# Kernel tuning notes

Measured on AMD Instinct MI355X. Metric: run time of the kernel, lower is better.

Reference implementation:

```python
import jax, jax.numpy as jnp
import numpy as np

HEADS = 8
DIM_HEAD = 64
SCALE = DIM_HEAD ** -0.5  # q scaling
EPS = 1e-5  # channel LayerNorm eps (float32)


def setup_inputs() -> dict:
    key = jax.random.key(0)
    ks = jax.random.split(key, 4)
    B, C, H, W = 8, 256, 64, 64
    hd = HEADS * DIM_HEAD  # 512
    x = jax.random.normal(ks[0], (B, C, H, W), dtype=jnp.float32)
    w_qkv = jax.random.normal(ks[1], (3 * hd, C), dtype=jnp.float32) * 0.02  # 1x1 conv, no bias
    w_out = jax.random.normal(ks[2], (C, hd), dtype=jnp.float32) * 0.02     # 1x1 conv
    b_out = jax.random.normal(ks[3], (C,), dtype=jnp.float32) * 0.02
    g_ln = jnp.ones((C,), dtype=jnp.float32)  # LayerNorm gamma
    return {"x": x, "w_qkv": w_qkv, "w_out": w_out, "b_out": b_out, "g_ln": g_ln}


def reference(x, w_qkv, w_out, b_out, g_ln):
    B, C, H, W = x.shape
    n = H * W
    hd = HEADS * DIM_HEAD
    # 1x1 conv == per-pixel matmul: [B,C,H,W] x [3hd,C] -> [B,3hd,H,W]
    qkv = jnp.einsum('bchw,oc->bohw', x, w_qkv).reshape(B, 3, HEADS, DIM_HEAD, n)
    q, k, v = qkv[:, 0], qkv[:, 1], qkv[:, 2]  # each [B,h,d,n]
    q = jax.nn.softmax(q, axis=-2) * SCALE      # softmax over head-dim d
    k = jax.nn.softmax(k, axis=-1)              # softmax over spatial n
    v = v / n
    context = jnp.einsum('bhdn,bhen->bhde', k, v)   # [B,h,d,e]
    out = jnp.einsum('bhde,bhdn->bhen', context, q)  # [B,h,e,n]
    out = out.reshape(B, hd, H, W)
    # to_out: 1x1 conv + bias, then channel-wise LayerNorm (gamma only)
    y = jnp.einsum('bchw,oc->bohw', out, w_out) + b_out[None, :, None, None]
    mean = jnp.mean(y, axis=1, keepdims=True)
    var = jnp.var(y, axis=1, keepdims=True)  # unbiased=False
    return (y - mean) * jax.lax.rsqrt(var + EPS) * g_ln[None, :, None, None]
```

## Files before the change

### kernel.cpp

```cpp
#include <hip/hip_runtime.h>
#include <stdint.h>


#define NB    8
#define CCH   256
#define NSP   4096
#define O3    1536
#define NH    8
#define DH    64
#define CSTR  136

typedef unsigned short u16;
typedef unsigned int   u32;
typedef __bf16 bf16;
typedef bf16  bf16x8 __attribute__((ext_vector_type(8)));
typedef float f32x4  __attribute__((ext_vector_type(4)));
typedef u16   u16x8  __attribute__((ext_vector_type(8)));
typedef u16   u16x4  __attribute__((ext_vector_type(4)));

__device__ __forceinline__ float b2f(u16 h) {
  union { u32 u; float f; } x; x.u = ((u32)h) << 16; return x.f;
}
__device__ __forceinline__ u16 f2b(float f) {
  union { float f; u32 u; } x; x.f = f;
  u32 r = x.u + 0x7fffu + ((x.u >> 16) & 1u);
  return (u16)(r >> 16);
}
__device__ __forceinline__ int detect_bf(const void* g) {
  return ((const u32*)g)[0] != 0x3F800000u;
}
__device__ __forceinline__ void ldg2lds16(const u16* g, u16* l) {
  __builtin_amdgcn_global_load_lds((const __attribute__((address_space(1))) void*)g,
                                   (__attribute__((address_space(3))) void*)l,
                                   16, 0, 0);
}

#define TSTR 68
__global__ __launch_bounds__(256) void k_prep(const void* __restrict__ xv,
                                              const void* __restrict__ wv,
                                              u16* __restrict__ xT,
                                              u16* __restrict__ Wb,
                                              float* __restrict__ S,
                                              const void* __restrict__ g_lnv) {
  const int isbf = detect_bf(g_lnv);
  const int t = threadIdx.x;
  if (blockIdx.z == 8) {
    const int tid = blockIdx.y * 64 + blockIdx.x;
    if (tid < 192) {
      const int idx = tid * 256 + t;
      const int row = idx >> 5, cu = idx & 31;
      int nr;
      if (row < 512)       nr = row;
      else if (row < 1024) nr = 512 + ((row - 512) >> 6) * 128 + (row & 63);
      else                 nr = 512 + ((row - 1024) >> 6) * 128 + 64 + (row & 63);
      const int didx = nr * 32 + cu;
      if (isbf) {
        reinterpret_cast<uint4*>(Wb)[didx] = reinterpret_cast<const uint4*>(wv)[idx];
      } else {
        float4 a = reinterpret_cast<const float4*>(wv)[idx * 2];
        float4 b = reinterpret_cast<const float4*>(wv)[idx * 2 + 1];
        ushort4 o0, o1;
        o0.x = f2b(a.x); o0.y = f2b(a.y); o0.z = f2b(a.z); o0.w = f2b(a.w);
        o1.x = f2b(b.x); o1.y = f2b(b.y); o1.z = f2b(b.z); o1.w = f2b(b.w);
        reinterpret_cast<ushort4*>(Wb)[didx * 2]     = o0;
        reinterpret_cast<ushort4*>(Wb)[didx * 2 + 1] = o1;
      }
    } else if (tid < 200) {
      reinterpret_cast<float2*>(S)[(tid - 192) * 256 + t] = (float2){0.f, 0.f};
    }
    return;
  }
  const int b = blockIdx.z, cb = blockIdx.y * 64, nb = blockIdx.x * 64;
  __shared__ u16 tile[64 * TSTR];
  if (isbf) {
    const u16* xb = (const u16*)xv;
#pragma unroll
    for (int rr = 0; rr < 2; ++rr) {
      const int u = t + 256 * rr;
      const int c = u >> 3, ch = u & 7;
      u16x8 v = *reinterpret_cast<const u16x8*>(
          xb + ((size_t)(b * CCH + cb + c) * NSP + nb + ch * 8));
      u16* dst = tile + c * TSTR + ch * 8;
      *reinterpret_cast<u16x4*>(dst)     = (u16x4){v[0], v[1], v[2], v[3]};
      *reinterpret_cast<u16x4*>(dst + 4) = (u16x4){v[4], v[5], v[6], v[7]};
    }
  } else {
    const float* xb = (const float*)xv;
#pragma unroll
    for (int rr = 0; rr < 4; ++rr) {
      const int u = t + 256 * rr;
      const int c = u >> 4, c4 = u & 15;
      float4 f = *reinterpret_cast<const float4*>(
          xb + ((size_t)(b * CCH + cb + c) * NSP + nb + c4 * 4));
      u16x4 o; o[0] = f2b(f.x); o[1] = f2b(f.y); o[2] = f2b(f.z); o[3] = f2b(f.w);
      *reinterpret_cast<u16x4*>(tile + c * TSTR + c4 * 4) = o;
    }
  }
  __syncthreads();
#pragma unroll
  for (int rr = 0; rr < 2; ++rr) {
    const int u = t + 256 * rr;
    const int n = u >> 3, cc = u & 7;
    u16x8 o;
#pragma unroll
    for (int e = 0; e < 8; ++e) o[e] = tile[(cc * 8 + e) * TSTR + n];
    *reinterpret_cast<u16x8*>(
        xT + ((size_t)(b * NSP + nb + n) * CCH + cb + cc * 8)) = o;
  }
}

__global__ __launch_bounds__(256) void k_kv_mfma(const u16* __restrict__ Wb,
                                                 const u16* __restrict__ xT,
                                                 float* __restrict__ S,
                                                 float* __restrict__ ctxp) {
  __shared__ __align__(16) u16 pool[64 * CSTR * 2];
  u16* As = pool;
  u16* Bs = pool + 4096;
  u16* ekS = pool;
  u16* vS  = pool + 64 * CSTR;

  const int b = blockIdx.z, h = blockIdx.y, n0 = blockIdx.x * 128;
  const int m0 = 512 + h * 128;
  const int t = threadIdx.x, w = t >> 6, l = t & 63;
  const int wm = (w >> 1) * 64, wn = (w & 1) * 64;
  const int fr = l & 15, quad = l >> 4;

  f32x4 acc[4][4];
#pragma unroll
  for (int i = 0; i < 4; ++i)
#pragma unroll
    for (int j = 0; j < 4; ++j) acc[i][j] = (f32x4){0.f, 0.f, 0.f, 0.f};

  {
    const u16* A = Wb;
    const u16* B = xT + (size_t)b * NSP * CCH;
    const int s0 = w * 2, s1 = s0 + 1;
    const int ra0 = s0 * 16 + (l >> 2);
    const int ra1 = s1 * 16 + (l >> 2);
    const int kc  = (l & 3) * 8;
    const int fq  = quad * 8;
    for (int k0 = 0; k0 < 256; k0 += 32) {
      ldg2lds16(A + (size_t)(m0 + ra0) * 256 + k0 + kc, As + s0 * 512);
      ldg2lds16(A + (size_t)(m0 + ra1) * 256 + k0 + kc, As + s1 * 512);
      ldg2lds16(B + (size_t)(n0 + ra0) * 256 + k0 + kc, Bs + s0 * 512);
      ldg2lds16(B + (size_t)(n0 + ra1) * 256 + k0 + kc, Bs + s1 * 512);
      asm volatile("s_waitcnt vmcnt(0)" ::: "memory");
      __syncthreads();
      bf16x8 af[4], bg[4];
#pragma unroll
      for (int i = 0; i < 4; ++i)
        af[i] = *reinterpret_cast<const bf16x8*>(As + (wm + i * 16 + fr) * 32 + fq);
#pragma unroll
      for (int j = 0; j < 4; ++j)
        bg[j] = *reinterpret_cast<const bf16x8*>(Bs + (wn + j * 16 + fr) * 32 + fq);
#pragma unroll
      for (int i = 0; i < 4; ++i)
#pragma unroll
        for (int j = 0; j < 4; ++j)
          acc[i][j] = __builtin_amdgcn_mfma_f32_16x16x32_bf16(af[i], bg[j], acc[i][j], 0, 0, 0);
      __syncthreads();
    }
  }

  {
    u16* dstT = (w < 2) ? ekS : vS;
#pragma unroll
    for (int i = 0; i < 4; ++i)
#pragma unroll
      for (int r = 0; r < 4; ++r) {
        const int row = i * 16 + quad * 4 + r;
#pragma unroll
        for (int j = 0; j < 4; ++j) {
          float v = acc[i][j][r];
          if (w < 2) v = __expf(v);
          dstT[row * CSTR + wn + j * 16 + fr] = f2b(v);
        }
      }
  }
  __syncthreads();

  {
    const int d = t >> 2, seg = t & 3;
    float s = 0.f;
    const u16* src = ekS + d * CSTR + seg * 32;
#pragma unroll
    for (int m = 0; m < 32; ++m) s += b2f(src[m]);
    s += __shfl_xor(s, 1);
    s += __shfl_xor(s, 2);
    if ((t & 3) == 0) atomicAdd(&S[b * 512 + h * 64 + d], s);
  }

  f32x4 c2[4];
#pragma unroll
  for (int j = 0; j < 4; ++j) c2[j] = (f32x4){0.f, 0.f, 0.f, 0.f};
#pragma unroll
  for (int k0 = 0; k0 < 128; k0 += 32) {
    bf16x8 af = *reinterpret_cast<const bf16x8*>(ekS + (w * 16 + fr) * CSTR + k0 + quad * 8);
#pragma unroll
    for (int j = 0; j < 4; ++j) {
      bf16x8 bg = *reinterpret_cast<const bf16x8*>(vS + (j * 16 + fr) * CSTR + k0 + quad * 8);
      c2[j] = __builtin_amdgcn_mfma_f32_16x16x32_bf16(af, bg, c2[j], 0, 0, 0);
    }
  }
  float* cb = ctxp + ((size_t)blockIdx.x * 64 + b * NH + h) * 4096;
#pragma unroll
  for (int j = 0; j < 4; ++j)
#pragma unroll
    for (int r = 0; r < 4; ++r)
      cb[(w * 16 + quad * 4 + r) * 64 + j * 16 + fr] = c2[j][r];
}

__global__ __launch_bounds__(256) void k_fold(const float* __restrict__ ctxp,
                                              const void* __restrict__ w_outv,
                                              const float* __restrict__ S,
                                              u16* __restrict__ Mb,
                                              const void* __restrict__ g_lnv) {
  const int isbf = detect_bf(g_lnv);
  const int h = blockIdx.x, b = blockIdx.y, ds = blockIdx.z * 16;
  const int t = threadIdx.x;
  __shared__ float ctxS[16][64];
  __shared__ float invS[16];
  if (t < 16) invS[t] = (1.0f / 4096.0f) / S[b * 512 + h * 64 + ds + t];
  const size_t bhoff = (size_t)(b * NH + h) * 4096 + (size_t)ds * 64;
#pragma unroll
  for (int i = 0; i < 4; ++i) {
    const int idx = t + 256 * i;
    float s = 0.f;
#pragma unroll
    for (int ch = 0; ch < 32; ++ch)
      s += ctxp[(size_t)ch * 64 * 4096 + bhoff + idx];
    ctxS[idx >> 6][idx & 63] = s;
  }
  float wrow[64];
  if (isbf) {
    const u16* wsrc = (const u16*)w_outv + (size_t)t * 512 + h * DH;
#pragma unroll
    for (int e4 = 0; e4 < 64; e4 += 4) {
      ushort4 u = *reinterpret_cast<const ushort4*>(wsrc + e4);
      wrow[e4 + 0] = b2f(u.x); wrow[e4 + 1] = b2f(u.y);
      wrow[e4 + 2] = b2f(u.z); wrow[e4 + 3] = b2f(u.w);
    }
  } else {
    const float* wsrc = (const float*)w_outv + (size_t)t * 512 + h * DH;
#pragma unroll
    for (int e4 = 0; e4 < 64; e4 += 4) {
      float4 f = *reinterpret_cast<const float4*>(wsrc + e4);
      wrow[e4 + 0] = f.x; wrow[e4 + 1] = f.y;
      wrow[e4 + 2] = f.z; wrow[e4 + 3] = f.w;
    }
  }
  __syncthreads();
  u16* dst = Mb + ((size_t)(b * CCH + t)) * 512 + h * DH + ds;
  for (int d = 0; d < 16; ++d) {
    float s = 0.f;
#pragma unroll
    for (int e = 0; e < 64; e += 4) {
      float4 c4 = *reinterpret_cast<const float4*>(&ctxS[d][e]);
      s += wrow[e] * c4.x + wrow[e + 1] * c4.y + wrow[e + 2] * c4.z + wrow[e + 3] * c4.w;
    }
    dst[d] = f2b(s * invS[d]);
  }
}

__global__ __launch_bounds__(512) void k_qmq_ln(const u16* __restrict__ Wb,
                                                const u16* __restrict__ xT,
                                                const u16* __restrict__ Mb,
                                                const void* __restrict__ b_outv,
                                                const void* __restrict__ g_lnv,
                                                void* __restrict__ outv) {
  __shared__ __align__(16) u16 qS[64 * 512];
  __shared__ __align__(16) u16 pool[18432];
  __shared__ float redS[8][4][16];
  __shared__ float redQ[8][4][16];
  __shared__ float gS[256], bS[256];

  const int isbf = detect_bf(g_lnv);
  const int b  = blockIdx.y;
  const int n0 = blockIdx.x * 64;
  const int t  = threadIdx.x, w = t >> 6, l = t & 63;
  const int fr = l & 15, quad = l >> 4;
  const int kcs = (((l & 3) ^ ((l >> 3) & 3)) * 8);
  const int fsw = (quad ^ ((fr >> 1) & 3)) * 8;

  if (t < 256) {
    gS[t] = isbf ? b2f(((const u16*)g_lnv)[t]) : ((const float*)g_lnv)[t];
    bS[t] = isbf ? b2f(((const u16*)b_outv)[t]) : ((const float*)b_outv)[t];
  }

  {
    u16* As = pool;
    u16* Bs = pool + 16384;
    f32x4 qa[4][4];
#pragma unroll
    for (int i = 0; i < 4; ++i)
#pragma unroll
      for (int j = 0; j < 4; ++j) qa[i][j] = (f32x4){0.f, 0.f, 0.f, 0.f};

    const u16* Bg = xT + (size_t)b * NSP * CCH;
    for (int k0 = 0; k0 < 256; k0 += 32) {
#pragma unroll
      for (int s = 0; s < 4; ++s) {
        const int row = w * 64 + s * 16 + (l >> 2);
        ldg2lds16(Wb + (size_t)row * 256 + k0 + kcs, As + (w * 64 + s * 16) * 32);
      }
      if (w < 4) {
        const int row = w * 16 + (l >> 2);
        ldg2lds16(Bg + (size_t)(n0 + row) * 256 + k0 + kcs, Bs + (w * 16) * 32);
      }
      asm volatile("s_waitcnt vmcnt(0)" ::: "memory");
      __syncthreads();
      bf16x8 af[4], bg[4];
#pragma unroll
      for (int i = 0; i < 4; ++i)
        af[i] = *reinterpret_cast<const bf16x8*>(As + (w * 64 + i * 16 + fr) * 32 + fsw);
#pragma unroll
      for (int j = 0; j < 4; ++j)
        bg[j] = *reinterpret_cast<const bf16x8*>(Bs + (j * 16 + fr) * 32 + fsw);
#pragma unroll
      for (int i = 0; i < 4; ++i)
#pragma unroll
        for (int j = 0; j < 4; ++j)
          qa[i][j] = __builtin_amdgcn_mfma_f32_16x16x32_bf16(af[i], bg[j], qa[i][j], 0, 0, 0);
      __syncthreads();
    }

#pragma unroll
    for (int j = 0; j < 4; ++j) {
      float s = 0.f;
#pragma unroll
      for (int i = 0; i < 4; ++i)
#pragma unroll
        for (int r = 0; r < 4; ++r) { qa[i][j][r] = __expf(qa[i][j][r]); s += qa[i][j][r]; }
      s += __shfl_xor(s, 16);
      s += __shfl_xor(s, 32);
      const float inv = 0.125f / s;
      const int n   = j * 16 + fr;
      const int swz = (n & 7) << 4;
#pragma unroll
      for (int i = 0; i < 4; ++i) {
        ushort4 o;
        o.x = f2b(qa[i][j][0] * inv); o.y = f2b(qa[i][j][1] * inv);
        o.z = f2b(qa[i][j][2] * inv); o.w = f2b(qa[i][j][3] * inv);
        const int hd2 = (w * 64 + i * 16 + quad * 4) * 2;
        *reinterpret_cast<ushort4*>(
            reinterpret_cast<char*>(qS) + ((n * 1024 + hd2) ^ swz)) = o;
      }
    }
  }
  __syncthreads();

  f32x4 acc[2][4];
#pragma unroll
  for (int i = 0; i < 2; ++i)
#pragma unroll
    for (int j = 0; j < 4; ++j) acc[i][j] = (f32x4){0.f, 0.f, 0.f, 0.f};

  {
    u16* Am = pool;
    const u16* Ag = Mb + (size_t)b * CCH * 512;
    for (int k0 = 0; k0 < 512; k0 += 32) {
#pragma unroll
      for (int s = 0; s < 2; ++s) {
        const int row = w * 32 + s * 16 + (l >> 2);
        ldg2lds16(Ag + (size_t)row * 512 + k0 + kcs, Am + (w * 32 + s * 16) * 32);
      }
      asm volatile("s_waitcnt vmcnt(0)" ::: "memory");
      __syncthreads();
      bf16x8 af[2], bg[4];
#pragma unroll
      for (int i = 0; i < 2; ++i)
        af[i] = *reinterpret_cast<const bf16x8*>(Am + (w * 32 + i * 16 + fr) * 32 + fsw);
#pragma unroll
      for (int j = 0; j < 4; ++j) {
        const int n = j * 16 + fr;
        const int byteoff = (n * 1024 + k0 * 2 + quad * 16) ^ ((n & 7) << 4);
        bg[j] = *reinterpret_cast<const bf16x8*>(
            reinterpret_cast<const char*>(qS) + byteoff);
      }
#pragma unroll
      for (int i = 0; i < 2; ++i)
#pragma unroll
        for (int j = 0; j < 4; ++j)
          acc[i][j] = __builtin_amdgcn_mfma_f32_16x16x32_bf16(af[i], bg[j], acc[i][j], 0, 0, 0);
      __syncthreads();
    }
  }

  float ps[4] = {}, pq[4] = {};
#pragma unroll
  for (int i = 0; i < 2; ++i)
#pragma unroll
    for (int r = 0; r < 4; ++r) {
      const int c = w * 32 + i * 16 + quad * 4 + r;
      const float bi = bS[c];
#pragma unroll
      for (int j = 0; j < 4; ++j) {
        acc[i][j][r] += bi;
        ps[j] += acc[i][j][r];
        pq[j] += acc[i][j][r] * acc[i][j][r];
      }
    }
#pragma unroll
  for (int j = 0; j < 4; ++j) {
    ps[j] += __shfl_xor(ps[j], 16); ps[j] += __shfl_xor(ps[j], 32);
    pq[j] += __shfl_xor(pq[j], 16); pq[j] += __shfl_xor(pq[j], 32);
  }
  if (quad == 0) {
#pragma unroll
    for (int j = 0; j < 4; ++j) { redS[w][j][fr] = ps[j]; redQ[w][j][fr] = pq[j]; }
  }
  __syncthreads();
  float mean[4], inv[4];
#pragma unroll
  for (int j = 0; j < 4; ++j) {
    float s = 0.f, q = 0.f;
#pragma unroll
    for (int g = 0; g < 8; ++g) { s += redS[g][j][fr]; q += redQ[g][j][fr]; }
    const float mn = s * (1.0f / 256.0f);
    const float vr = q * (1.0f / 256.0f) - mn * mn;
    mean[j] = mn;
    inv[j] = rsqrtf(vr + 1e-5f);
  }

#pragma unroll
  for (int i = 0; i < 2; ++i)
#pragma unroll
    for (int r = 0; r < 4; ++r) {
      const int c = w * 32 + i * 16 + quad * 4 + r;
      const float g = gS[c];
#pragma unroll
      for (int j = 0; j < 4; ++j) {
        const int col = n0 + j * 16 + fr;
        const float o = (acc[i][j][r] - mean[j]) * inv[j] * g;
        const size_t idx = ((size_t)b * CCH + c) * NSP + col;
        if (isbf) ((u16*)outv)[idx] = f2b(o);
        else      ((float*)outv)[idx] = o;
      }
    }
}

extern "C" void kernel_launch(void* const* d_in, const int* in_sizes, int n_in,
                              void* d_out, int out_size, void* d_ws, size_t ws_size,
                              hipStream_t stream) {
  (void)in_sizes; (void)n_in; (void)out_size; (void)ws_size;
  const void* x     = d_in[0];
  const void* w_qkv = d_in[1];
  const void* w_out = d_in[2];
  const void* b_out = d_in[3];
  const void* g_ln  = d_in[4];

  char* ws = (char*)d_ws;
  u16*   Wb   = (u16*)(ws + 256);
  float* S    = (float*)(ws + 851968);
  u16*   xT   = (u16*)(ws + 1048576);
  float* ctxp = (float*)(ws + 17825792);
  u16*   Mb   = (u16*)(ws + 51380224);

  k_prep    <<<dim3(64, 4, 9),  256, 0, stream>>>(x, w_qkv, xT, Wb, S, g_ln);
  k_kv_mfma <<<dim3(32, NH, NB),256, 0, stream>>>(Wb, xT, S, ctxp);
  k_fold    <<<dim3(NH, NB, 4), 256, 0, stream>>>(ctxp, w_out, S, Mb, g_ln);
  k_qmq_ln  <<<dim3(64, NB),    512, 0, stream>>>(Wb, xT, Mb, b_out, g_ln, d_out);
}
```

Baseline: 176.9 us.

## Double-buffer LDS tiles in both GEMM phases and prefetch second-phase operand

Doubles the shared pool so the q-projection GEMM and the context GEMM each double-buffer their global-to-LDS tiles, using partial vmcnt waits so the next tile's loads overlap the current tile's MFMAs. The second GEMM's K step grows from 32 to 64 with a new XOR swizzle, and its first tile is issued before the softmax epilogue so that load overlaps the exp/normalize work. The larger LDS footprint may lower occupancy, and the hand-counted vmcnt values and raw s_barrier calls have to match the number of outstanding loads exactly.

Measured after the change: 171.3 us. 3.2% less time.

```diff
diff --git a/kernel.cpp b/kernel.cpp
--- a/kernel.cpp
+++ b/kernel.cpp
@@ -269,7 +269,7 @@
                                                 const void* __restrict__ g_lnv,
                                                 void* __restrict__ outv) {
   __shared__ __align__(16) u16 qS[64 * 512];
-  __shared__ __align__(16) u16 pool[18432];
+  __shared__ __align__(16) u16 pool[36864];
   __shared__ float redS[8][4][16];
   __shared__ float redQ[8][4][16];
   __shared__ float gS[256], bS[256];
@@ -287,64 +287,98 @@
     bS[t] = isbf ? b2f(((const u16*)b_outv)[t]) : ((const float*)b_outv)[t];
   }
 
+  const u16* Bg = xT + (size_t)b * NSP * CCH;
+  const u16* Ag = Mb + (size_t)b * CCH * 512;
+
+  f32x4 qa[4][4];
+#pragma unroll
+  for (int i = 0; i < 4; ++i)
+#pragma unroll
+    for (int j = 0; j < 4; ++j) qa[i][j] = (f32x4){0.f, 0.f, 0.f, 0.f};
+
   {
-    u16* As = pool;
-    u16* Bs = pool + 16384;
-    f32x4 qa[4][4];
-#pragma unroll
-    for (int i = 0; i < 4; ++i)
-#pragma unroll
-      for (int j = 0; j < 4; ++j) qa[i][j] = (f32x4){0.f, 0.f, 0.f, 0.f};
-
-    const u16* Bg = xT + (size_t)b * NSP * CCH;
-    for (int k0 = 0; k0 < 256; k0 += 32) {
+    {
+      u16* As0 = pool; u16* Bs0 = pool + 16384;
 #pragma unroll
       for (int s = 0; s < 4; ++s) {
         const int row = w * 64 + s * 16 + (l >> 2);
-        ldg2lds16(Wb + (size_t)row * 256 + k0 + kcs, As + (w * 64 + s * 16) * 32);
+        ldg2lds16(Wb + (size_t)row * 256 + kcs, As0 + (w * 64 + s * 16) * 32);
       }
       if (w < 4) {
-        const int row = w * 16 + (l >> 2);
-        ldg2lds16(Bg + (size_t)(n0 + row) * 256 + k0 + kcs, Bs + (w * 16) * 32);
-      }
-      asm volatile("s_waitcnt vmcnt(0)" ::: "memory");
-      __syncthreads();
+        const int row = n0 + w * 16 + (l >> 2);
+        ldg2lds16(Bg + (size_t)row * 256 + kcs, Bs0 + (w * 16) * 32);
+      }
+    }
+    int cur = 0;
+    for (int k0 = 0; k0 < 256; k0 += 32) {
+      const int last = (k0 + 32 >= 256);
+      if (!last) {
+        u16* Asn = pool + (cur ^ 1) * 18432;
+        u16* Bsn = Asn + 16384;
+        const int kn = k0 + 32;
+#pragma unroll
+        for (int s = 0; s < 4; ++s) {
+          const int row = w * 64 + s * 16 + (l >> 2);
+          ldg2lds16(Wb + (size_t)row * 256 + kn + kcs, Asn + (w * 64 + s * 16) * 32);
+        }
+        if (w < 4) {
+          const int row = n0 + w * 16 + (l >> 2);
+          ldg2lds16(Bg + (size_t)row * 256 + kn + kcs, Bsn + (w * 16) * 32);
+        }
+        if (w < 4) asm volatile("s_waitcnt vmcnt(5)" ::: "memory");
+        else       asm volatile("s_waitcnt vmcnt(4)" ::: "memory");
+      } else {
+        asm volatile("s_waitcnt vmcnt(0)" ::: "memory");
+      }
+      __builtin_amdgcn_s_barrier();
+      const u16* Asc = pool + cur * 18432;
+      const u16* Bsc = Asc + 16384;
       bf16x8 af[4], bg[4];
 #pragma unroll
       for (int i = 0; i < 4; ++i)
-        af[i] = *reinterpret_cast<const bf16x8*>(As + (w * 64 + i * 16 + fr) * 32 + fsw);
+        af[i] = *reinterpret_cast<const bf16x8*>(Asc + (w * 64 + i * 16 + fr) * 32 + fsw);
 #pragma unroll
       for (int j = 0; j < 4; ++j)
-        bg[j] = *reinterpret_cast<const bf16x8*>(Bs + (j * 16 + fr) * 32 + fsw);
+        bg[j] = *reinterpret_cast<const bf16x8*>(Bsc + (j * 16 + fr) * 32 + fsw);
 #pragma unroll
       for (int i = 0; i < 4; ++i)
 #pragma unroll
         for (int j = 0; j < 4; ++j)
           qa[i][j] = __builtin_amdgcn_mfma_f32_16x16x32_bf16(af[i], bg[j], qa[i][j], 0, 0, 0);
-      __syncthreads();
-    }
-
-#pragma unroll
-    for (int j = 0; j < 4; ++j) {
-      float s = 0.f;
-#pragma unroll
-      for (int i = 0; i < 4; ++i)
-#pragma unroll
-        for (int r = 0; r < 4; ++r) { qa[i][j][r] = __expf(qa[i][j][r]); s += qa[i][j][r]; }
-      s += __shfl_xor(s, 16);
-      s += __shfl_xor(s, 32);
-      const float inv = 0.125f / s;
-      const int n   = j * 16 + fr;
-      const int swz = (n & 7) << 4;
-#pragma unroll
-      for (int i = 0; i < 4; ++i) {
-        ushort4 o;
-        o.x = f2b(qa[i][j][0] * inv); o.y = f2b(qa[i][j][1] * inv);
-        o.z = f2b(qa[i][j][2] * inv); o.w = f2b(qa[i][j][3] * inv);
-        const int hd2 = (w * 64 + i * 16 + quad * 4) * 2;
-        *reinterpret_cast<ushort4*>(
-            reinterpret_cast<char*>(qS) + ((n * 1024 + hd2) ^ swz)) = o;
-      }
+      __builtin_amdgcn_s_barrier();
+      cur ^= 1;
+    }
+  }
+
+  {
+    const int srck = ((l & 7) ^ ((l >> 3) & 7)) * 8;
+#pragma unroll
+    for (int s = 0; s < 4; ++s) {
+      const int r0 = w * 32 + s * 8;
+      ldg2lds16(Ag + (size_t)(r0 + (l >> 3)) * 512 + srck, pool + r0 * 64);
+    }
+  }
+
+#pragma unroll
+  for (int j = 0; j < 4; ++j) {
+    float s = 0.f;
+#pragma unroll
+    for (int i = 0; i < 4; ++i)
+#pragma unroll
+      for (int r = 0; r < 4; ++r) { qa[i][j][r] = __expf(qa[i][j][r]); s += qa[i][j][r]; }
+    s += __shfl_xor(s, 16);
+    s += __shfl_xor(s, 32);
+    const float inv = 0.125f / s;
+    const int n   = j * 16 + fr;
+    const int swz = (n & 7) << 4;
+#pragma unroll
+    for (int i = 0; i < 4; ++i) {
+      ushort4 o;
+      o.x = f2b(qa[i][j][0] * inv); o.y = f2b(qa[i][j][1] * inv);
+      o.z = f2b(qa[i][j][2] * inv); o.w = f2b(qa[i][j][3] * inv);
+      const int hd2 = (w * 64 + i * 16 + quad * 4) * 2;
+      *reinterpret_cast<ushort4*>(
+          reinterpret_cast<char*>(qS) + ((n * 1024 + hd2) ^ swz)) = o;
     }
   }
   __syncthreads();
@@ -356,33 +390,53 @@
     for (int j = 0; j < 4; ++j) acc[i][j] = (f32x4){0.f, 0.f, 0.f, 0.f};
 
   {
-    u16* Am = pool;
-    const u16* Ag = Mb + (size_t)b * CCH * 512;
-    for (int k0 = 0; k0 < 512; k0 += 32) {
-#pragma unroll
-      for (int s = 0; s < 2; ++s) {
-        const int row = w * 32 + s * 16 + (l >> 2);
-        ldg2lds16(Ag + (size_t)row * 512 + k0 + kcs, Am + (w * 32 + s * 16) * 32);
-      }
-      asm volatile("s_waitcnt vmcnt(0)" ::: "memory");
-      __syncthreads();
-      bf16x8 af[2], bg[4];
-#pragma unroll
-      for (int i = 0; i < 2; ++i)
-        af[i] = *reinterpret_cast<const bf16x8*>(Am + (w * 32 + i * 16 + fr) * 32 + fsw);
+    const int srck = ((l & 7) ^ ((l >> 3) & 7)) * 8;
+    int cur = 0;
+    for (int k0 = 0; k0 < 512; k0 += 64) {
+      const int last = (k0 + 64 >= 512);
+      if (!last) {
+        u16* Amn = pool + (cur ^ 1) * 16384;
+        const int kn = k0 + 64;
+#pragma unroll
+        for (int s = 0; s < 4; ++s) {
+          const int r0 = w * 32 + s * 8;
+          ldg2lds16(Ag + (size_t)(r0 + (l >> 3)) * 512 + kn + srck, Amn + r0 * 64);
+        }
+        asm volatile("s_waitcnt vmcnt(4)" ::: "memory");
+      } else {
+        asm volatile("s_waitcnt vmcnt(0)" ::: "memory");
+      }
+      __builtin_amdgcn_s_barrier();
+      const u16* Amc = pool + cur * 16384;
+      bf16x8 af0[2], af1[2], bg0[4], bg1[4];
+      const int c0 = (quad ^ (fr & 7)) * 8;
+      const int c1 = ((4 + quad) ^ (fr & 7)) * 8;
+#pragma unroll
+      for (int i = 0; i < 2; ++i) {
+        const int rb = (w * 32 + i * 16 + fr) * 64;
+        af0[i] = *reinterpret_cast<const bf16x8*>(Amc + rb + c0);
+        af1[i] = *reinterpret_cast<const bf16x8*>(Amc + rb + c1);
+      }
 #pragma unroll
       for (int j = 0; j < 4; ++j) {
         const int n = j * 16 + fr;
-        const int byteoff = (n * 1024 + k0 * 2 + quad * 16) ^ ((n & 7) << 4);
-        bg[j] = *reinterpret_cast<const bf16x8*>(
-            reinterpret_cast<const char*>(qS) + byteoff);
+        const int o0 = (n * 1024 + k0 * 2 + quad * 16) ^ ((n & 7) << 4);
+        const int o1 = (n * 1024 + (k0 + 32) * 2 + quad * 16) ^ ((n & 7) << 4);
+        bg0[j] = *reinterpret_cast<const bf16x8*>(reinterpret_cast<const char*>(qS) + o0);
+        bg1[j] = *reinterpret_cast<const bf16x8*>(reinterpret_cast<const char*>(qS) + o1);
       }
 #pragma unroll
       for (int i = 0; i < 2; ++i)
 #pragma unroll
         for (int j = 0; j < 4; ++j)
-          acc[i][j] = __builtin_amdgcn_mfma_f32_16x16x32_bf16(af[i], bg[j], acc[i][j], 0, 0, 0);
-      __syncthreads();
+          acc[i][j] = __builtin_amdgcn_mfma_f32_16x16x32_bf16(af0[i], bg0[j], acc[i][j], 0, 0, 0);
+#pragma unroll
+      for (int i = 0; i < 2; ++i)
+#pragma unroll
+        for (int j = 0; j < 4; ++j)
+          acc[i][j] = __builtin_amdgcn_mfma_f32_16x16x32_bf16(af1[i], bg1[j], acc[i][j], 0, 0, 0);
+      __builtin_amdgcn_s_barrier();
+      cur ^= 1;
     }
   }
 
```
